# Kernel tuning notes

Hardware: AMD Instinct MI355X
Metric: run time of the kernel (lower is better)

## Reference

```python
import jax, jax.numpy as jnp
import numpy as np

DIM = 192; HEADS = 6; WIN = 8; HIDDEN = int(DIM * 2.66); EPS = 1e-5

def dct_matrix(n):
    # DCT-II orthonormal matrix, matches get_dctMatrix(n, n)
    i = np.arange(n)[:, None]; j = np.arange(n)[None, :]
    M = np.cos(np.pi * i * (2 * j + 1) / (2 * n)) * np.sqrt(2.0 / n)
    M[0, :] = np.sqrt(1.0 / n)
    return jnp.asarray(M, dtype=jnp.float32)

def layernorm_c(x, w, b):
    # WithBias LayerNorm over channel dim of BCHW (restormer to_3d/to_4d style)
    mu = x.mean(axis=1, keepdims=True)
    var = ((x - mu) ** 2).mean(axis=1, keepdims=True)
    return (x - mu) / jnp.sqrt(var + EPS) * w[None, :, None, None] + b[None, :, None, None]

def conv1x1(x, w, b=None):
    y = jnp.einsum('oc,bchw->bohw', w, x)
    return y if b is None else y + b[None, :, None, None]

def dwconv3x3(x, w):
    return jax.lax.conv_general_dilated(x, w, (1, 1), ((1, 1), (1, 1)),
        dimension_numbers=('NCHW', 'OIHW', 'NCHW'), feature_group_count=x.shape[1])

def l2norm(x):
    n = jnp.sqrt(jnp.sum(x * x, axis=-1, keepdims=True))
    return x / jnp.maximum(n, 1e-12)

def window_channel_attn(qkv, temperature):
    # 'b (z head c) (h1 h) (w1 w) -> z (b h1 w1) head c (h w)'
    b, _, H, W = qkv.shape
    cph = DIM // HEADS
    h1, w1 = H // WIN, W // WIN
    t = qkv.reshape(b, 3, HEADS, cph, h1, WIN, w1, WIN)
    t = t.transpose(1, 0, 4, 6, 2, 3, 5, 7).reshape(3, b * h1 * w1, HEADS, cph, WIN * WIN)
    q, k, v = t[0], t[1], t[2]
    q = l2norm(q); k = l2norm(k)
    attn = jnp.einsum('nhce,nhde->nhcd', q, k) * temperature[None]  # channel x channel per window
    attn = jax.nn.softmax(attn, axis=-1)
    out = jnp.einsum('nhcd,nhde->nhce', attn, v)
    out = out.reshape(b, h1, w1, HEADS, cph, WIN, WIN)
    out = out.transpose(0, 3, 4, 1, 5, 2, 6).reshape(b, DIM, H, W)
    return out

def forward(x, norm1_w, norm1_b, w_qkv, w_dw, temperature, w_proj, b_proj,
            norm2_w, norm2_b, w_in, w_dwf, w_out):
    B, C, H, W = x.shape
    Mh = dct_matrix(H); Mw = dct_matrix(W)
    # attention branch in DCT domain
    y = layernorm_c(x, norm1_w, norm1_b)
    y = jnp.einsum('ph,bchw->bcpw', Mh, y)      # dct2dx: Mh @ y @ Mw.T
    y = jnp.einsum('bcpw,qw->bcpq', y, Mw)
    qkv = dwconv3x3(conv1x1(y, w_qkv), w_dw)
    a = window_channel_attn(qkv, temperature)
    a = conv1x1(a, w_proj, b_proj)
    a = jnp.einsum('bcpq,qw->bcpw', a, Mw)      # idct2dx: Mh.T @ a @ Mw
    a = jnp.einsum('bcpw,ph->bchw', a, Mh)
    x1 = x + a
    # gated-dconv FFN branch
    z = layernorm_c(x1, norm2_w, norm2_b)
    f = dwconv3x3(conv1x1(z, w_in), w_dwf)
    f1, f2 = jnp.split(f, 2, axis=1)
    f = jax.nn.gelu(f1, approximate=False) * f2
    f = conv1x1(f, w_out)
    return x1 + f

def setup_inputs() -> dict:
    key = jax.random.key(0)
    ks = jax.random.split(key, 8)
    B, C, H, W = 2, DIM, 192, 192
    s = 0.02
    return {
        'x': jax.random.normal(ks[0], (B, C, H, W), jnp.float32),
        'norm1_w': jnp.ones((C,), jnp.float32),
        'norm1_b': jnp.zeros((C,), jnp.float32),
        'w_qkv': jax.random.normal(ks[1], (3 * C, C), jnp.float32) * s,
        'w_dw': jax.random.normal(ks[2], (3 * C, 1, 3, 3), jnp.float32) * s,
        'temperature': jnp.ones((HEADS, 1, 1), jnp.float32) / np.float32(np.sqrt(C)),
        'w_proj': jax.random.normal(ks[3], (C, C), jnp.float32) * s,
        'b_proj': jnp.zeros((C,), jnp.float32),
        'norm2_w': jnp.ones((C,), jnp.float32),
        'norm2_b': jnp.zeros((C,), jnp.float32),
        'w_in': jax.random.normal(ks[4], (2 * HIDDEN, C), jnp.float32) * s,
        'w_dwf': jax.random.normal(ks[5], (2 * HIDDEN, 1, 3, 3), jnp.float32) * s,
        'w_out': jax.random.normal(ks[6], (C, HIDDEN), jnp.float32) * s,
    }

def reference(x, norm1_w, norm1_b, w_qkv, w_dw, temperature, w_proj, b_proj,
              norm2_w, norm2_b, w_in, w_dwf, w_out):
    return forward(x, norm1_w, norm1_b, w_qkv, w_dw, temperature, w_proj, b_proj,
                   norm2_w, norm2_b, w_in, w_dwf, w_out)
```

## Files before the change

kernel.cpp:

```cpp
#include <hip/hip_runtime.h>
#include <hip/hip_bf16.h>

typedef __hip_bfloat16 bft;
typedef __attribute__((ext_vector_type(8))) short bf16x8;
typedef __attribute__((ext_vector_type(4))) float f32x4;

#define BLK 256
static constexpr int Cc = 192;
static constexpr int L  = 192;
static constexpr int S  = 36864;
static constexpr int Bn = 2;
static constexpr int HID = 510;
static constexpr int CH = 64;
static constexpr int FTR = (CH + 2) * L;
static constexpr int GTR = CH * L;
static constexpr double PI_D = 3.141592653589793238462643383279502884;

__device__ __forceinline__ float ldf(const float* p) { return *p; }
__device__ __forceinline__ float ldf(const bft* p)   { return __bfloat162float(*p); }
__device__ __forceinline__ void  stf(float* p, float v) { *p = v; }
__device__ __forceinline__ void  stf(bft* p, float v)   { *p = __float2bfloat16(v); }
__device__ __forceinline__ unsigned short f2bfu(float f) {
    bft h = __float2bfloat16(f);
    return *reinterpret_cast<const unsigned short*>(&h);
}
__device__ __forceinline__ unsigned short bfu(const bft* p) {
    return *reinterpret_cast<const unsigned short*>(p);
}
__device__ __forceinline__ float bu2f(unsigned short u) {
    unsigned int x = (unsigned int)u << 16;
    return __uint_as_float(x);
}
__device__ __forceinline__ bf16x8 ld8(const unsigned short* p) {
    union { unsigned int u[4]; bf16x8 v; } t;
    const unsigned int* q = reinterpret_cast<const unsigned int*>(p);
    t.u[0] = q[0]; t.u[1] = q[1]; t.u[2] = q[2]; t.u[3] = q[3];
    return t.v;
}

__global__ __launch_bounds__(BLK) void k_dct_init(bft* __restrict__ dctb,
                                                  bft* __restrict__ dctTb) {
    int idx = blockIdx.x * BLK + threadIdx.x;
    if (idx >= L * L) return;
    int p = idx / L, h = idx - p * L;
    double v = (p == 0) ? sqrt(1.0 / L)
                        : cos(PI_D * p * (2 * h + 1) / (2.0 * L)) * sqrt(2.0 / L);
    bft bv = __float2bfloat16((float)v);
    dctb[p * L + h] = bv;
    dctTb[h * L + p] = bv;
}

__global__ __launch_bounds__(BLK) void k_cvt(const float* __restrict__ src,
                                             bft* __restrict__ dst,
                                             int Mr, int Kr, int Kp) {
    int idx = blockIdx.x * BLK + threadIdx.x;
    int m = idx / Kp, k = idx - m * Kp;
    float v = (m < Mr && k < Kr) ? src[(size_t)m * Kr + k] : 0.f;
    dst[idx] = __float2bfloat16(v);
}

__global__ __launch_bounds__(BLK) void k_cvt_ffn(const float* __restrict__ src,
                                                 bft* __restrict__ dst) {
    int idx = blockIdx.x * BLK + threadIdx.x;
    int m = idx / Cc, k = idx - m * Cc;
    float v = 0.f;
    if (m < 510) v = src[(size_t)m * Cc + k];
    else if (m >= 512 && m < 1022) v = src[(size_t)(m - 2) * Cc + k];
    dst[idx] = __float2bfloat16(v);
}

template <typename TI, bool TRANS>
__global__ __launch_bounds__(BLK) void k_lnt(const TI* __restrict__ x,
                                             const float* __restrict__ w,
                                             const float* __restrict__ b,
                                             bft* __restrict__ out,
                                             long zI, long zO) {
    __shared__ float t[192][65];
    __shared__ float mus[64], rs[64];
    const int tid = threadIdx.x;
    const int s0 = blockIdx.x * 64;
    const TI* xp = x + (size_t)blockIdx.y * zI;
    if constexpr (sizeof(TI) == 4) {
        for (int id = tid; id < 192 * 16; id += BLK) {
            int c = id >> 4, q = id & 15;
            float4 v = *reinterpret_cast<const float4*>(
                (const float*)xp + (size_t)c * S + s0 + q * 4);
            t[c][q * 4 + 0] = v.x; t[c][q * 4 + 1] = v.y;
            t[c][q * 4 + 2] = v.z; t[c][q * 4 + 3] = v.w;
        }
    } else {
        for (int id = tid; id < 192 * 8; id += BLK) {
            int c = id >> 3, q = id & 7;
            uint4 raw = *reinterpret_cast<const uint4*>(
                (const bft*)xp + (size_t)c * S + s0 + q * 8);
            const unsigned short* u = reinterpret_cast<const unsigned short*>(&raw);
#pragma unroll
            for (int e = 0; e < 8; ++e) t[c][q * 8 + e] = bu2f(u[e]);
        }
    }
    __syncthreads();
    {
        int px = tid >> 2, g = tid & 3;
        float sum = 0.f, sq = 0.f;
#pragma unroll
        for (int j = 0; j < 48; ++j) {
            float v = t[g * 48 + j][px];
            sum += v; sq += v * v;
        }
        sum += __shfl_xor(sum, 1); sum += __shfl_xor(sum, 2);
        sq  += __shfl_xor(sq, 1);  sq  += __shfl_xor(sq, 2);
        float mu = sum * (1.f / Cc);
        float var = sq * (1.f / Cc) - mu * mu;
        float r = rsqrtf(var + 1e-5f);
        if (g == 0) { mus[px] = mu; rs[px] = r; }
    }
    __syncthreads();
    bft* op = out + (size_t)blockIdx.y * zO;
    if constexpr (!TRANS) {
        for (int id = tid; id < 192 * 8; id += BLK) {
            int c = id >> 3, q = id & 7;
            float wc = w[c], bc = b[c];
            unsigned short v8[8];
#pragma unroll
            for (int e = 0; e < 8; ++e) {
                int px = q * 8 + e;
                v8[e] = f2bfu((t[c][px] - mus[px]) * rs[px] * wc + bc);
            }
            *reinterpret_cast<uint4*>(op + (size_t)c * S + s0 + q * 8) =
                *reinterpret_cast<uint4*>(v8);
        }
    } else {
#pragma unroll
        for (int qq = 0; qq < 3; ++qq) {
            for (int id = tid; id < 512; id += BLK) {
                int s = id >> 3, qlo = id & 7;
                int q = qq * 8 + qlo;
                float mu = mus[s], r = rs[s];
                unsigned short v8[8];
#pragma unroll
                for (int e = 0; e < 8; ++e) {
                    int c = q * 8 + e;
                    v8[e] = f2bfu((t[c][s] - mu) * r * w[c] + b[c]);
                }
                *reinterpret_cast<uint4*>(op + (size_t)(s0 + s) * Cc + q * 8) =
                    *reinterpret_cast<uint4*>(v8);
            }
        }
    }
}

__global__ __launch_bounds__(BLK) void k_tr(const bft* __restrict__ in,
                                            bft* __restrict__ out, long z) {
    __shared__ unsigned short t[32][72];
    const int tid = threadIdx.x;
    const int s0 = blockIdx.x * 64, c0 = blockIdx.y * 32;
    const bft* ip = in + (size_t)blockIdx.z * z;
    bft* op = out + (size_t)blockIdx.z * z;
    {
        int c = tid >> 3, sc = (tid & 7) * 8;
        *reinterpret_cast<uint4*>(&t[c][sc]) =
            *reinterpret_cast<const uint4*>(ip + (size_t)(c0 + c) * S + s0 + sc);
    }
    __syncthreads();
    {
        int s = tid >> 2, cc = (tid & 3) * 8;
        unsigned short v[8];
#pragma unroll
        for (int q = 0; q < 8; ++q) v[q] = t[cc + q][s];
        *reinterpret_cast<uint4*>(op + (size_t)(s0 + s) * Cc + c0 + cc) =
            *reinterpret_cast<uint4*>(v);
    }
}

__global__ __launch_bounds__(BLK) void k_w2s(const bft* __restrict__ src,
                                             bft* __restrict__ dst,
                                             long zI, long zO) {
    __shared__ unsigned short t[192][100];
    const int tid = threadIdx.x;
    const int hh = blockIdx.x;
    const int ch0 = blockIdx.y * 96;
    const int bz = blockIdx.z;
    const int h1 = hh >> 3, ii = hh & 7;
    const bft* ip = src + (size_t)bz * zI;
    for (int id = tid; id < 192 * 12; id += BLK) {
        int r = id / 12, q = id - r * 12;
        int w1 = r >> 3, jj = r & 7;
        int s = (h1 * 24 + w1) * 64 + ii * 8 + jj;
        *reinterpret_cast<uint4*>(&t[r][q * 8]) =
            *reinterpret_cast<const uint4*>(ip + (size_t)s * Cc + ch0 + q * 8);
    }
    __syncthreads();
    bft* op = dst + (size_t)bz * zO;
    for (int id = tid; id < 96 * 24; id += BLK) {
        int c = id / 24, q = id - c * 24;
        unsigned short v[8];
#pragma unroll
        for (int e = 0; e < 8; ++e) v[e] = t[q * 8 + e][c];
        *reinterpret_cast<uint4*>(op + (size_t)(ch0 + c) * S + (size_t)hh * L + q * 8) =
            *reinterpret_cast<uint4*>(v);
    }
}

template <int WR, int WC, int FM, int FN, int KSTEP, int BMODE, int OMODE,
          bool HASBIAS, bool BIASN, bool HASRES, typename OutT, typename ResT>
__global__ __launch_bounds__(256) void k_mm(
    const bft* __restrict__ A, int strideA, int Mreal, long zA,
    const bft* __restrict__ B, int strideB, long zB,
    OutT* __restrict__ Out, int strideO, long zO,
    const float* __restrict__ bias,
    const ResT* __restrict__ Res, long zR,
    int K, int rlo, int rhi) {
    constexpr int BM = WR * FM * 16, BN = WC * FN * 16;
    constexpr int AV = KSTEP / 8;
    __shared__ unsigned short lds[(BM + BN) * (KSTEP + 8)];
    unsigned short (*Al)[KSTEP + 8] =
        reinterpret_cast<unsigned short(*)[KSTEP + 8]>(lds);
    unsigned short (*Bl)[KSTEP + 8] =
        reinterpret_cast<unsigned short(*)[KSTEP + 8]>(lds + BM * (KSTEP + 8));
    const int tid = threadIdx.x;
    const int n0 = blockIdx.x * BN, m0 = blockIdx.y * BM, bz = blockIdx.z;
    const int lane = tid & 63, wv = tid >> 6;
    const int wr = wv / WC, wc = wv % WC;
    const int l15 = lane & 15, l4 = lane >> 4;
    f32x4 acc[FM][FN] = {};

    const bft* Ab = A + (size_t)bz * zA;
    const bft* Bb = B + (size_t)bz * zB;

    for (int k0 = 0; k0 < K; k0 += KSTEP) {
        for (int id = tid; id < BM * AV; id += 256) {
            int row = id / AV, kc = (id % AV) * 8;
            int gm = m0 + row; if (gm >= Mreal) gm = Mreal - 1;
            *reinterpret_cast<uint4*>(&Al[row][kc]) =
                *reinterpret_cast<const uint4*>(Ab + (size_t)gm * strideA + k0 + kc);
        }
        for (int id = tid; id < BN * AV; id += 256) {
            int row = id / AV, kc = (id % AV) * 8;
            int gn = n0 + row;
            uint4 val;
            if constexpr (BMODE == 2) {
                val = *reinterpret_cast<const uint4*>(
                    Bb + (size_t)gn * strideB + k0 + kc);
            } else {
                if (gn >= rlo && gn < rhi)
                    val = *reinterpret_cast<const uint4*>(
                        Bb + (size_t)gn * strideB + k0 + kc);
                else
                    val = make_uint4(0, 0, 0, 0);
            }
            *reinterpret_cast<uint4*>(&Bl[row][kc]) = val;
        }
        __syncthreads();
#pragma unroll
        for (int kk = 0; kk < KSTEP / 32; ++kk) {
            bf16x8 af[FM], bf[FN];
#pragma unroll
            for (int i = 0; i < FM; ++i)
                af[i] = *reinterpret_cast<const bf16x8*>(
                    &Al[wr * FM * 16 + i * 16 + l15][kk * 32 + l4 * 8]);
#pragma unroll
            for (int j = 0; j < FN; ++j)
                bf[j] = *reinterpret_cast<const bf16x8*>(
                    &Bl[wc * FN * 16 + j * 16 + l15][kk * 32 + l4 * 8]);
#pragma unroll
            for (int i = 0; i < FM; ++i)
#pragma unroll
                for (int j = 0; j < FN; ++j)
                    acc[i][j] = __builtin_amdgcn_mfma_f32_16x16x32_bf16(
                        af[i], bf[j], acc[i][j], 0, 0, 0);
        }
        __syncthreads();
    }
    if constexpr (OMODE == 3) {
        constexpr int OST = BM + 8;
        unsigned short* Ol = lds;
#pragma unroll
        for (int i = 0; i < FM; ++i) {
            int mB = wr * FM * 16 + i * 16 + l4 * 4;
#pragma unroll
            for (int j = 0; j < FN; ++j) {
                int n = wc * FN * 16 + j * 16 + l15;
                unsigned short v[4];
#pragma unroll
                for (int r = 0; r < 4; ++r) v[r] = f2bfu(acc[i][j][r]);
                *reinterpret_cast<uint2*>(&Ol[n * OST + mB]) =
                    *reinterpret_cast<uint2*>(v);
            }
        }
        __syncthreads();
        constexpr int TPR = (BM == 128) ? 2 : 1;
        int row = tid / TPR;
        int seg = (TPR == 2) ? (tid & 1) * 64 : 0;
        if (row < BN) {
            bft* dst = (bft*)Out + (size_t)bz * zO
                     + (size_t)(n0 + row) * strideO + m0 + seg;
            const unsigned short* src = &Ol[row * OST + seg];
#pragma unroll
            for (int q = 0; q < 8; ++q)
                *reinterpret_cast<uint4*>(dst + q * 8) =
                    *reinterpret_cast<const uint4*>(src + q * 8);
        }
        return;
    }
#pragma unroll
    for (int i = 0; i < FM; ++i) {
        int mB = m0 + wr * FM * 16 + i * 16 + l4 * 4;
#pragma unroll
        for (int j = 0; j < FN; ++j) {
            int n = n0 + wc * FN * 16 + j * 16 + l15;
#pragma unroll
            for (int r = 0; r < 4; ++r) {
                int m = mB + r;
                if (m >= Mreal) continue;
                float vv = acc[i][j][r];
                if constexpr (HASBIAS) vv += BIASN ? bias[n] : bias[m];
                size_t idx;
                if constexpr (OMODE == 0)
                    idx = (size_t)bz * zO + (size_t)m * strideO + n;
                else {
                    int win = n >> 6, e = n & 63;
                    int hh = ((win / 24) << 3) + (e >> 3);
                    int ww = ((win % 24) << 3) + (e & 7);
                    idx = (size_t)bz * zO + (size_t)m * S + (size_t)hh * L + ww;
                }
                if constexpr (HASRES) vv += ldf(Res + ((OMODE == 0)
                                  ? ((size_t)bz * zR + (size_t)m * strideO + n) : idx));
                stf(Out + idx, vv);
            }
        }
    }
}

__global__ __launch_bounds__(BLK) void k_dwconv(const bft* __restrict__ in,
                                                long inZ,
                                                const float* __restrict__ wt,
                                                bft* __restrict__ out,
                                                long outZ) {
    int t = blockIdx.x * BLK + threadIdx.x;
    int ch2 = t / (S / 8);
    int rem = t - ch2 * (S / 8);
    int b = ch2 / Cc, ch = ch2 - b * Cc;
    int h = rem / 24, wb = (rem - h * 24) * 8;
    const float* wp = wt + (size_t)ch * 9;
    const bft* ip = in + (size_t)b * inZ + (size_t)ch * S;
    float acc[8] = {};
#pragma unroll
    for (int dy = -1; dy <= 1; ++dy) {
        int hh = h + dy;
        if (hh < 0 || hh >= L) continue;
        const bft* rp = ip + hh * L + wb;
        float e[10];
        uint4 mid = *reinterpret_cast<const uint4*>(rp);
        const unsigned short* ms = reinterpret_cast<const unsigned short*>(&mid);
#pragma unroll
        for (int q = 0; q < 8; ++q) e[q + 1] = bu2f(ms[q]);
        e[0] = (wb > 0) ? ldf(rp - 1) : 0.f;
        e[9] = (wb + 8 < L) ? ldf(rp + 8) : 0.f;
        float c0 = wp[(dy + 1) * 3], c1 = wp[(dy + 1) * 3 + 1], c2 = wp[(dy + 1) * 3 + 2];
#pragma unroll
        for (int q = 0; q < 8; ++q)
            acc[q] += c0 * e[q] + c1 * e[q + 1] + c2 * e[q + 2];
    }
    int win = (h >> 3) * 24 + (wb >> 3);
    int e0 = (h & 7) * 8;
    unsigned short ov[8];
#pragma unroll
    for (int q = 0; q < 8; ++q) ov[q] = f2bfu(acc[q]);
    *reinterpret_cast<uint4*>(out + (size_t)b * outZ + (size_t)ch * S + win * 64 + e0) =
        *reinterpret_cast<uint4*>(ov);
}

__global__ __launch_bounds__(256) void k_attn_mfma(
    const bft* __restrict__ QW, long zQ,
    const bft* __restrict__ KW, long zK,
    const bft* __restrict__ VW, long zV,
    const float* __restrict__ temp,
    bft* __restrict__ outp, long zO) {
    __shared__ unsigned short qls[4][32 * 66];
    __shared__ unsigned short kls[4][32 * 66];
    __shared__ unsigned short vls[4][32 * 66];
    __shared__ float rqs[4][32], rks[4][32];
    const int tid = threadIdx.x;
    const int wv = tid >> 6, lane = tid & 63;
    const int win = blockIdx.x * 4 + wv;
    const int hd = blockIdx.y;
    const int bz = blockIdx.z;
    const int l15 = lane & 15, l4 = lane >> 4;
    unsigned short* ql = qls[wv];
    unsigned short* kl = kls[wv];
    unsigned short* vl = vls[wv];
    const size_t base = (size_t)(hd * 32) * S + (size_t)win * 64;

#pragma unroll
    for (int i = 0; i < 4; ++i) {
        int c = i * 8 + (lane >> 3), e0 = (lane & 7) * 8;
        size_t g = base + (size_t)c * S + e0;
        uint4 vq = *reinterpret_cast<const uint4*>(QW + (size_t)bz * zQ + g);
        uint4 vk = *reinterpret_cast<const uint4*>(KW + (size_t)bz * zK + g);
        uint4 vvv = *reinterpret_cast<const uint4*>(VW + (size_t)bz * zV + g);
        unsigned int* dq = reinterpret_cast<unsigned int*>(&ql[c * 66 + e0]);
        unsigned int* dk = reinterpret_cast<unsigned int*>(&kl[c * 66 + e0]);
        unsigned int* dv = reinterpret_cast<unsigned int*>(&vl[c * 66 + e0]);
        dq[0] = vq.x; dq[1] = vq.y; dq[2] = vq.z; dq[3] = vq.w;
        dk[0] = vk.x; dk[1] = vk.y; dk[2] = vk.z; dk[3] = vk.w;
        dv[0] = vvv.x; dv[1] = vvv.y; dv[2] = vvv.z; dv[3] = vvv.w;
    }
    __syncthreads();
    {
        int row = lane & 31;
        const unsigned short* src = (lane < 32) ? ql : kl;
        float s = 0.f;
#pragma unroll
        for (int w = 0; w < 32; ++w) {
            unsigned int d = *reinterpret_cast<const unsigned int*>(&src[row * 66 + 2 * w]);
            float a = bu2f((unsigned short)(d & 0xffff));
            float b = bu2f((unsigned short)(d >> 16));
            s += a * a + b * b;
        }
        float r = 1.f / fmaxf(sqrtf(s), 1e-12f);
        if (lane < 32) rqs[wv][row] = r; else rks[wv][row] = r;
    }
    __syncthreads();
    f32x4 at[2][2] = {};
#pragma unroll
    for (int ks = 0; ks < 2; ++ks) {
        bf16x8 aq[2], bk[2];
#pragma unroll
        for (int i = 0; i < 2; ++i)
            aq[i] = ld8(&ql[(i * 16 + l15) * 66 + ks * 32 + l4 * 8]);
#pragma unroll
        for (int j = 0; j < 2; ++j)
            bk[j] = ld8(&kl[(j * 16 + l15) * 66 + ks * 32 + l4 * 8]);
#pragma unroll
        for (int i = 0; i < 2; ++i)
#pragma unroll
            for (int j = 0; j < 2; ++j)
                at[i][j] = __builtin_amdgcn_mfma_f32_16x16x32_bf16(
                    aq[i], bk[j], at[i][j], 0, 0, 0);
    }
    float tpr = temp[hd];
    float rk0 = rks[wv][l15] * tpr, rk1 = rks[wv][16 + l15] * tpr;
    float pr[2][2][4];
#pragma unroll
    for (int i = 0; i < 2; ++i)
#pragma unroll
        for (int r = 0; r < 4; ++r) {
            int c = i * 16 + l4 * 4 + r;
            float rq = rqs[wv][c];
            float v0 = at[i][0][r] * rq * rk0;
            float v1 = at[i][1][r] * rq * rk1;
            float mx = fmaxf(v0, v1);
#pragma unroll
            for (int m = 1; m < 16; m <<= 1) mx = fmaxf(mx, __shfl_xor(mx, m));
            v0 = __expf(v0 - mx);
            v1 = __expf(v1 - mx);
            float sm = v0 + v1;
#pragma unroll
            for (int m = 1; m < 16; m <<= 1) sm += __shfl_xor(sm, m);
            float inv = 1.f / sm;
            pr[i][0][r] = v0 * inv;
            pr[i][1][r] = v1 * inv;
        }
    __syncthreads();
    unsigned short* pl = ql;
#pragma unroll
    for (int i = 0; i < 2; ++i)
#pragma unroll
        for (int j = 0; j < 2; ++j)
#pragma unroll
            for (int r = 0; r < 4; ++r)
                pl[(i * 16 + l4 * 4 + r) * 34 + j * 16 + l15] = f2bfu(pr[i][j][r]);
    __syncthreads();
    bf16x8 ap[2];
#pragma unroll
    for (int i = 0; i < 2; ++i)
        ap[i] = ld8(&pl[(i * 16 + l15) * 34 + l4 * 8]);
    f32x4 o[2][4] = {};
#pragma unroll
    for (int j = 0; j < 4; ++j) {
        unsigned short tv[8];
#pragma unroll
        for (int q = 0; q < 8; ++q)
            tv[q] = vl[(l4 * 8 + q) * 66 + j * 16 + l15];
        bf16x8 bv = *reinterpret_cast<bf16x8*>(tv);
#pragma unroll
        for (int i = 0; i < 2; ++i)
            o[i][j] = __builtin_amdgcn_mfma_f32_16x16x32_bf16(ap[i], bv, o[i][j], 0, 0, 0);
    }
#pragma unroll
    for (int i = 0; i < 2; ++i)
#pragma unroll
        for (int j = 0; j < 4; ++j) {
            int e = j * 16 + l15, cl = i * 16 + l4 * 4;
            unsigned short v[4];
#pragma unroll
            for (int r = 0; r < 4; ++r) v[r] = f2bfu(o[i][j][r]);
            unsigned short* row = ((e < 32) ? kl : vl) + (e & 31) * 40 + cl;
            *reinterpret_cast<uint2*>(row) = *reinterpret_cast<uint2*>(v);
        }
    {
        const unsigned short* row = ((lane < 32) ? kl : vl) + (lane & 31) * 40;
        bft* dst = outp + (size_t)bz * zO + (size_t)(win * 64 + lane) * Cc + hd * 32;
#pragma unroll
        for (int q = 0; q < 4; ++q)
            *reinterpret_cast<uint4*>(dst + q * 8) =
                *reinterpret_cast<const uint4*>(row + q * 8);
    }
}

__global__ __launch_bounds__(BLK) void k_gateT(const bft* __restrict__ fTg,
                                               const float* __restrict__ wt,
                                               bft* __restrict__ gTg) {
    __shared__ float w1s[64][9];
    __shared__ float w2s[64][9];
    const int tid = threadIdx.x;
    const int cbase = blockIdx.y * 64;
    const bft* fT = fTg + (size_t)blockIdx.z * FTR * 1024;
    bft* gT = gTg + (size_t)blockIdx.z * GTR * 512;
    for (int id = tid; id < 576; id += BLK) {
        int cl = id / 9, k = id - cl * 9;
        int c = cbase + cl;
        w1s[cl][k] = (c < HID) ? wt[(size_t)c * 9 + k] : 0.f;
        w2s[cl][k] = (c < HID) ? wt[(size_t)(c + HID) * 9 + k] : 0.f;
    }
    __syncthreads();
    int px = blockIdx.x * 32 + (tid >> 3);
    int cgl = (tid & 7) * 8;
    int hc = px / L, w = px - hc * L;
    float a1[8] = {}, a2[8] = {};
#pragma unroll
    for (int dy = 0; dy < 3; ++dy) {
#pragma unroll
        for (int dx = 0; dx < 3; ++dx) {
            int ww = w + dx - 1;
            if (ww < 0 || ww >= L) continue;
            size_t frow = (size_t)((hc + dy) * L + ww) * 1024 + cbase + cgl;
            uint4 u1 = *reinterpret_cast<const uint4*>(fT + frow);
            uint4 u2 = *reinterpret_cast<const uint4*>(fT + frow + 512);
            const unsigned short* e1 = reinterpret_cast<const unsigned short*>(&u1);
            const unsigned short* e2 = reinterpret_cast<const unsigned short*>(&u2);
            int k = dy * 3 + dx;
#pragma unroll
            for (int j = 0; j < 8; ++j) {
                a1[j] += w1s[cgl + j][k] * bu2f(e1[j]);
                a2[j] += w2s[cgl + j][k] * bu2f(e2[j]);
            }
        }
    }
    unsigned short ov[8];
#pragma unroll
    for (int j = 0; j < 8; ++j) {
        float ge = 0.5f * a1[j] * (1.f + erff(a1[j] * 0.70710678118654752f));
        ov[j] = f2bfu(ge * a2[j]);
    }
    *reinterpret_cast<uint4*>(gT + (size_t)px * 512 + cbase + cgl) =
        *reinterpret_cast<uint4*>(ov);
}

extern "C" void kernel_launch(void* const* d_in, const int* in_sizes, int n_in,
                              void* d_out, int out_size, void* d_ws, size_t ws_size,
                              hipStream_t stream) {
    const float* x      = (const float*)d_in[0];
    const float* n1w    = (const float*)d_in[1];
    const float* n1b    = (const float*)d_in[2];
    const float* w_qkv  = (const float*)d_in[3];
    const float* w_dw   = (const float*)d_in[4];
    const float* temp   = (const float*)d_in[5];
    const float* w_proj = (const float*)d_in[6];
    const float* b_proj = (const float*)d_in[7];
    const float* n2w    = (const float*)d_in[8];
    const float* n2b    = (const float*)d_in[9];
    const float* w_in   = (const float*)d_in[10];
    const float* w_dwf  = (const float*)d_in[11];
    const float* w_out  = (const float*)d_in[12];
    float* outp = (float*)d_out;

    const long CS = (long)Cc * S;
    const size_t DCT_B = 147456;
    const size_t BUF_B = (size_t)Bn * CS * 2;
    const size_t QKV_B = (size_t)Bn * 3 * CS * 2;
    const size_t WB_B  = 884736;
    const size_t NEED  = DCT_B + 3 * BUF_B + QKV_B + WB_B;
    if (ws_size < NEED) return;

    char* p = (char*)d_ws;
    bft* dctb  = (bft*)p;
    bft* dctTb = dctb + L * L;
    p += DCT_B;
    bft* X1    = (bft*)p;                  p += BUF_B;
    bft* PbB   = (bft*)p;                  p += BUF_B;
    bft* QbB   = (bft*)p;                  p += BUF_B;
    bft* QKV   = (bft*)p;                  p += QKV_B;
    bft* w_qkv_b = (bft*)p;
    bft* w_proj_b = w_qkv_b + 576 * 192;
    bft* w_in_b  = w_proj_b + 192 * 192;
    bft* w_out_b = w_in_b + 1024 * 192;
    bft* fT = QKV;
    bft* gT = QKV + (size_t)Bn * FTR * 1024;
    bft* attnT = QKV + CS;

    k_dct_init<<<144, BLK, 0, stream>>>(dctb, dctTb);
    k_cvt<<<432, BLK, 0, stream>>>(w_qkv, w_qkv_b, 576, 192, 192);
    k_cvt<<<144, BLK, 0, stream>>>(w_proj, w_proj_b, 192, 192, 192);
    k_cvt_ffn<<<768, BLK, 0, stream>>>(w_in, w_in_b);
    k_cvt<<<384, BLK, 0, stream>>>(w_out, w_out_b, 192, 510, 512);

    k_lnt<float, false><<<dim3(S / 64, Bn), BLK, 0, stream>>>(x, n1w, n1b, PbB, CS, CS);
    k_mm<2, 2, 2, 6, 64, 2, 3, false, false, false, bft, float><<<dim3(1, 3, Bn * Cc), 256, 0, stream>>>(
        PbB, L, L, S,  dctb, L, 0,  QbB, L, S,  nullptr, nullptr, 0,  L, 0, 0);
    k_mm<2, 2, 2, 6, 64, 2, 3, false, false, false, bft, float><<<dim3(1, 3, Bn * Cc), 256, 0, stream>>>(
        QbB, L, L, S,  dctb, L, 0,  PbB, L, S,  nullptr, nullptr, 0,  L, 0, 0);
    k_tr<<<dim3(576, 6, Bn), BLK, 0, stream>>>(PbB, QbB, CS);
    k_mm<2, 2, 4, 4, 64, 2, 0, false, false, false, bft, float><<<dim3(288, 5, Bn), 256, 0, stream>>>(
        w_qkv_b, Cc, 576, 0,  QbB, Cc, CS,  QKV, S, 3 * CS,  nullptr, nullptr, 0,  Cc, 0, 0);
    k_dwconv<<<6912, BLK, 0, stream>>>(QKV, 3 * CS, w_dw, PbB, CS);
    k_dwconv<<<6912, BLK, 0, stream>>>(QKV + CS, 3 * CS, w_dw + Cc * 9, QbB, CS);
    k_dwconv<<<6912, BLK, 0, stream>>>(QKV + 2 * CS, 3 * CS, w_dw + 2 * Cc * 9, QKV, 3 * CS);
    k_attn_mfma<<<dim3(144, 6, Bn), 256, 0, stream>>>(
        PbB, CS, QbB, CS, QKV, 3 * CS, temp, attnT, 3 * CS);
    k_mm<2, 2, 2, 6, 64, 2, 0, true, true, false, bft, float><<<dim3(1, 576, Bn), 256, 0, stream>>>(
        attnT, Cc, S, 3 * CS,  w_proj_b, Cc, 0,  PbB, Cc, CS,  b_proj, (const float*)nullptr, 0,  Cc, 0, 0);
    k_w2s<<<dim3(192, 2, Bn), BLK, 0, stream>>>(PbB, QbB, CS, CS);
    k_mm<2, 2, 2, 6, 64, 2, 3, false, false, false, bft, float><<<dim3(1, 3, Bn * Cc), 256, 0, stream>>>(
        QbB, L, L, S,  dctTb, L, 0,  PbB, L, S,  nullptr, nullptr, 0,  L, 0, 0);
    k_mm<2, 2, 2, 6, 64, 2, 0, false, false, true, bft, float><<<dim3(1, 3, Bn * Cc), 256, 0, stream>>>(
        dctTb, L, L, 0,  PbB, L, S,  X1, L, S,  nullptr, x, S,  L, 0, 0);

    k_lnt<bft, true><<<dim3(S / 64, Bn), BLK, 0, stream>>>(X1, n2w, n2b, QbB, CS, CS);
    for (int ck = 0; ck < 3; ++ck) {
        int h0 = ck * CH;
        long off = (long)(h0 - 1) * L;
        int rlo = (h0 == 0) ? L : 0;
        int rhi = (h0 == 2 * CH) ? (FTR - L) : FTR;
        k_mm<2, 2, 4, 4, 64, 4, 3, false, false, false, bft, float><<<dim3(99, 8, Bn), 256, 0, stream>>>(
            w_in_b, Cc, 1024, 0,  QbB + off * Cc, Cc, CS,  fT, 1024, (long)FTR * 1024,
            nullptr, nullptr, 0,  Cc, rlo, rhi);
        k_gateT<<<dim3(GTR / 32, 8, Bn), BLK, 0, stream>>>(fT, w_dwf, gT);
        k_mm<2, 2, 2, 4, 64, 2, 0, false, false, true, float, bft><<<dim3(96, 3, Bn), 256, 0, stream>>>(
            w_out_b, 512, 192, 0,  gT, 512, (long)GTR * 512,
            outp + (size_t)h0 * L, S, CS,
            nullptr, X1 + (size_t)h0 * L, CS,  512, 0, 0);
    }
}
```

Measured before the change: 753.9 us.

## Swap GEMM operand roles so pixels map to M with LDS-staged transposed epilogues

```diff
diff --git a/kernel.cpp b/kernel.cpp
--- a/kernel.cpp
+++ b/kernel.cpp
@@ -202,7 +202,8 @@
 }
 
 template <int WR, int WC, int FM, int FN, int KSTEP, int BMODE, int OMODE,
-          bool HASBIAS, bool BIASN, bool HASRES, typename OutT, typename ResT>
+          bool AMASK, bool HASBIAS, bool BIASN, bool HASRES,
+          typename OutT, typename ResT>
 __global__ __launch_bounds__(256) void k_mm(
     const bft* __restrict__ A, int strideA, int Mreal, long zA,
     const bft* __restrict__ B, int strideB, long zB,
@@ -212,7 +213,11 @@
     int K, int rlo, int rhi) {
     constexpr int BM = WR * FM * 16, BN = WC * FN * 16;
     constexpr int AV = KSTEP / 8;
-    __shared__ unsigned short lds[(BM + BN) * (KSTEP + 8)];
+    constexpr int KL = (BM + BN) * (KSTEP + 8);
+    constexpr int RST = (OMODE == 3 || OMODE == 4) ? BN * (BM + 8)
+                      : (OMODE == 5 ? BM * (BN + 8) : 0);
+    constexpr int LDSZ = (KL > RST) ? KL : RST;
+    __shared__ unsigned short lds[LDSZ];
     unsigned short (*Al)[KSTEP + 8] =
         reinterpret_cast<unsigned short(*)[KSTEP + 8]>(lds);
     unsigned short (*Bl)[KSTEP + 8] =
@@ -230,25 +235,24 @@
     for (int k0 = 0; k0 < K; k0 += KSTEP) {
         for (int id = tid; id < BM * AV; id += 256) {
             int row = id / AV, kc = (id % AV) * 8;
-            int gm = m0 + row; if (gm >= Mreal) gm = Mreal - 1;
-            *reinterpret_cast<uint4*>(&Al[row][kc]) =
-                *reinterpret_cast<const uint4*>(Ab + (size_t)gm * strideA + k0 + kc);
+            int gm = m0 + row;
+            if constexpr (AMASK) {
+                uint4 val = make_uint4(0, 0, 0, 0);
+                if (gm >= rlo && gm < rhi)
+                    val = *reinterpret_cast<const uint4*>(
+                        Ab + (size_t)gm * strideA + k0 + kc);
+                *reinterpret_cast<uint4*>(&Al[row][kc]) = val;
+            } else {
+                if (gm >= Mreal) gm = Mreal - 1;
+                *reinterpret_cast<uint4*>(&Al[row][kc]) =
+                    *reinterpret_cast<const uint4*>(Ab + (size_t)gm * strideA + k0 + kc);
+            }
         }
         for (int id = tid; id < BN * AV; id += 256) {
             int row = id / AV, kc = (id % AV) * 8;
-            int gn = n0 + row;
-            uint4 val;
-            if constexpr (BMODE == 2) {
-                val = *reinterpret_cast<const uint4*>(
-                    Bb + (size_t)gn * strideB + k0 + kc);
-            } else {
-                if (gn >= rlo && gn < rhi)
-                    val = *reinterpret_cast<const uint4*>(
-                        Bb + (size_t)gn * strideB + k0 + kc);
-                else
-                    val = make_uint4(0, 0, 0, 0);
-            }
-            *reinterpret_cast<uint4*>(&Bl[row][kc]) = val;
+            *reinterpret_cast<uint4*>(&Bl[row][kc]) =
+                *reinterpret_cast<const uint4*>(
+                    Bb + (size_t)(n0 + row) * strideB + k0 + kc);
         }
         __syncthreads();
 #pragma unroll
@@ -271,7 +275,7 @@
         }
         __syncthreads();
     }
-    if constexpr (OMODE == 3) {
+    if constexpr (OMODE == 3 || OMODE == 4) {
         constexpr int OST = BM + 8;
         unsigned short* Ol = lds;
 #pragma unroll
@@ -288,12 +292,62 @@
             }
         }
         __syncthreads();
-        constexpr int TPR = (BM == 128) ? 2 : 1;
-        int row = tid / TPR;
-        int seg = (TPR == 2) ? (tid & 1) * 64 : 0;
-        if (row < BN) {
+        constexpr int TPR = BM / 64;
+        for (int row = tid / TPR; row < BN; row += 256 / TPR) {
+            int seg = (tid % TPR) * 64;
+            const unsigned short* src = &Ol[row * OST + seg];
+            if constexpr (OMODE == 3) {
+                bft* dst = (bft*)Out + (size_t)bz * zO
+                         + (size_t)(n0 + row) * strideO + m0 + seg;
+#pragma unroll
+                for (int q = 0; q < 8; ++q)
+                    *reinterpret_cast<uint4*>(dst + q * 8) =
+                        *reinterpret_cast<const uint4*>(src + q * 8);
+            } else {
+                float* dst = (float*)Out + (size_t)bz * zO
+                           + (size_t)(n0 + row) * strideO + m0 + seg;
+                const bft* res = (const bft*)Res + (size_t)bz * zR
+                               + (size_t)(n0 + row) * strideO + m0 + seg;
+#pragma unroll
+                for (int q = 0; q < 8; ++q) {
+                    uint4 lv = *reinterpret_cast<const uint4*>(src + q * 8);
+                    uint4 rv = *reinterpret_cast<const uint4*>(res + q * 8);
+                    const unsigned short* le =
+                        reinterpret_cast<const unsigned short*>(&lv);
+                    const unsigned short* re =
+                        reinterpret_cast<const unsigned short*>(&rv);
+                    float o[8];
+#pragma unroll
+                    for (int e = 0; e < 8; ++e) o[e] = bu2f(le[e]) + bu2f(re[e]);
+                    *reinterpret_cast<float4*>(dst + q * 8) =
+                        make_float4(o[0], o[1], o[2], o[3]);
+                    *reinterpret_cast<float4*>(dst + q * 8 + 4) =
+                        make_float4(o[4], o[5], o[6], o[7]);
+                }
+            }
+        }
+        return;
+    }
+    if constexpr (OMODE == 5) {
+        constexpr int OST = BN + 8;
+        unsigned short* Ol = lds;
+#pragma unroll
+        for (int i = 0; i < FM; ++i) {
+            int mB = wr * FM * 16 + i * 16 + l4 * 4;
+#pragma unroll
+            for (int j = 0; j < FN; ++j) {
+                int n = wc * FN * 16 + j * 16 + l15;
+#pragma unroll
+                for (int r = 0; r < 4; ++r)
+                    Ol[(mB + r) * OST + n] = f2bfu(acc[i][j][r]);
+            }
+        }
+        __syncthreads();
+        constexpr int TPR = BN / 64;
+        for (int row = tid / TPR; row < BM; row += 256 / TPR) {
+            int seg = (tid % TPR) * 64;
             bft* dst = (bft*)Out + (size_t)bz * zO
-                     + (size_t)(n0 + row) * strideO + m0 + seg;
+                     + (size_t)(m0 + row) * strideO + n0 + seg;
             const unsigned short* src = &Ol[row * OST + seg];
 #pragma unroll
             for (int q = 0; q < 8; ++q)
@@ -606,24 +660,24 @@
     k_cvt<<<384, BLK, 0, stream>>>(w_out, w_out_b, 192, 510, 512);
 
     k_lnt<float, false><<<dim3(S / 64, Bn), BLK, 0, stream>>>(x, n1w, n1b, PbB, CS, CS);
-    k_mm<2, 2, 2, 6, 64, 2, 3, false, false, false, bft, float><<<dim3(1, 3, Bn * Cc), 256, 0, stream>>>(
+    k_mm<2, 2, 2, 6, 64, 2, 3, false, false, false, false, bft, float><<<dim3(1, 3, Bn * Cc), 256, 0, stream>>>(
         PbB, L, L, S,  dctb, L, 0,  QbB, L, S,  nullptr, nullptr, 0,  L, 0, 0);
-    k_mm<2, 2, 2, 6, 64, 2, 3, false, false, false, bft, float><<<dim3(1, 3, Bn * Cc), 256, 0, stream>>>(
+    k_mm<2, 2, 2, 6, 64, 2, 3, false, false, false, false, bft, float><<<dim3(1, 3, Bn * Cc), 256, 0, stream>>>(
         QbB, L, L, S,  dctb, L, 0,  PbB, L, S,  nullptr, nullptr, 0,  L, 0, 0);
     k_tr<<<dim3(576, 6, Bn), BLK, 0, stream>>>(PbB, QbB, CS);
-    k_mm<2, 2, 4, 4, 64, 2, 0, false, false, false, bft, float><<<dim3(288, 5, Bn), 256, 0, stream>>>(
-        w_qkv_b, Cc, 576, 0,  QbB, Cc, CS,  QKV, S, 3 * CS,  nullptr, nullptr, 0,  Cc, 0, 0);
+    k_mm<2, 2, 4, 6, 64, 2, 3, false, false, false, false, bft, float><<<dim3(3, 288, Bn), 256, 0, stream>>>(
+        QbB, Cc, S, CS,  w_qkv_b, Cc, 0,  QKV, S, 3 * CS,  nullptr, nullptr, 0,  Cc, 0, 0);
     k_dwconv<<<6912, BLK, 0, stream>>>(QKV, 3 * CS, w_dw, PbB, CS);
     k_dwconv<<<6912, BLK, 0, stream>>>(QKV + CS, 3 * CS, w_dw + Cc * 9, QbB, CS);
     k_dwconv<<<6912, BLK, 0, stream>>>(QKV + 2 * CS, 3 * CS, w_dw + 2 * Cc * 9, QKV, 3 * CS);
     k_attn_mfma<<<dim3(144, 6, Bn), 256, 0, stream>>>(
         PbB, CS, QbB, CS, QKV, 3 * CS, temp, attnT, 3 * CS);
-    k_mm<2, 2, 2, 6, 64, 2, 0, true, true, false, bft, float><<<dim3(1, 576, Bn), 256, 0, stream>>>(
+    k_mm<2, 2, 2, 6, 64, 2, 0, false, true, true, false, bft, float><<<dim3(1, 576, Bn), 256, 0, stream>>>(
         attnT, Cc, S, 3 * CS,  w_proj_b, Cc, 0,  PbB, Cc, CS,  b_proj, (const float*)nullptr, 0,  Cc, 0, 0);
     k_w2s<<<dim3(192, 2, Bn), BLK, 0, stream>>>(PbB, QbB, CS, CS);
-    k_mm<2, 2, 2, 6, 64, 2, 3, false, false, false, bft, float><<<dim3(1, 3, Bn * Cc), 256, 0, stream>>>(
+    k_mm<2, 2, 2, 6, 64, 2, 3, false, false, false, false, bft, float><<<dim3(1, 3, Bn * Cc), 256, 0, stream>>>(
         QbB, L, L, S,  dctTb, L, 0,  PbB, L, S,  nullptr, nullptr, 0,  L, 0, 0);
-    k_mm<2, 2, 2, 6, 64, 2, 0, false, false, true, bft, float><<<dim3(1, 3, Bn * Cc), 256, 0, stream>>>(
+    k_mm<2, 2, 2, 6, 64, 2, 0, false, false, false, true, bft, float><<<dim3(1, 3, Bn * Cc), 256, 0, stream>>>(
         dctTb, L, L, 0,  PbB, L, S,  X1, L, S,  nullptr, x, S,  L, 0, 0);
 
     k_lnt<bft, true><<<dim3(S / 64, Bn), BLK, 0, stream>>>(X1, n2w, n2b, QbB, CS, CS);
@@ -632,12 +686,12 @@
         long off = (long)(h0 - 1) * L;
         int rlo = (h0 == 0) ? L : 0;
         int rhi = (h0 == 2 * CH) ? (FTR - L) : FTR;
-        k_mm<2, 2, 4, 4, 64, 4, 3, false, false, false, bft, float><<<dim3(99, 8, Bn), 256, 0, stream>>>(
-            w_in_b, Cc, 1024, 0,  QbB + off * Cc, Cc, CS,  fT, 1024, (long)FTR * 1024,
+        k_mm<2, 2, 4, 4, 64, 2, 5, true, false, false, false, bft, float><<<dim3(8, 99, Bn), 256, 0, stream>>>(
+            QbB + off * Cc, Cc, FTR, CS,  w_in_b, Cc, 0,  fT, 1024, (long)FTR * 1024,
             nullptr, nullptr, 0,  Cc, rlo, rhi);
         k_gateT<<<dim3(GTR / 32, 8, Bn), BLK, 0, stream>>>(fT, w_dwf, gT);
-        k_mm<2, 2, 2, 4, 64, 2, 0, false, false, true, float, bft><<<dim3(96, 3, Bn), 256, 0, stream>>>(
-            w_out_b, 512, 192, 0,  gT, 512, (long)GTR * 512,
+        k_mm<2, 2, 4, 6, 64, 2, 4, false, false, false, true, float, bft><<<dim3(1, 96, Bn), 256, 0, stream>>>(
+            gT, 512, GTR, (long)GTR * 512,  w_out_b, 512, 0,
             outp + (size_t)h0 * L, S, CS,
             nullptr, X1 + (size_t)h0 * L, CS,  512, 0, 0);
     }
```

Result: slower. 825.8 us (+9.5%).
